# Performance work log

Hardware: AMD Instinct MI355X
Metric: run time of the kernel (lower is better)

Reference implementation:

```python
import jax, jax.numpy as jnp
import numpy as np


def setup_inputs() -> dict:
    key = jax.random.key(0)
    k1, k2, k3 = jax.random.split(key, 3)
    N, K, d, d_out = 100000, 32, 64, 64
    x = jax.random.normal(k1, (N, d), dtype=jnp.float32)
    edge_index = jax.random.randint(k2, (N, K), 0, N, dtype=jnp.int64)
    W = jax.random.normal(k3, (2 * d, d_out), dtype=jnp.float32) * (1.0 / np.sqrt(2 * d))
    b = jnp.zeros((d_out,), dtype=jnp.float32)
    return {"x": x, "edge_index": edge_index, "W": W, "b": b}


def reference(x, edge_index, W, b):
    # x: [N, d], edge_index: [N, K] dense neighbor indices
    x_j = x[edge_index]                                  # [N, K, d] gather
    # concat([x_i, x_j - x_i]) then max over K. The x_i half is constant over K,
    # so its max is x itself; max of the diff half computed directly (same math,
    # avoids materializing the [N, K, 2d] concat).
    diff_max = jnp.max(x_j - x[:, None, :], axis=1)      # [N, d]
    h = jnp.concatenate([x, diff_max], axis=-1)          # [N, 2d]
    return h @ W + b                                     # [N, d_out]
```

## Files before the change

### kernel.cpp

```cpp
#include <hip/hip_runtime.h>
#include <hip/hip_bf16.h>
#include <cstdint>


typedef __attribute__((ext_vector_type(8))) short short8;
typedef __attribute__((ext_vector_type(4))) float f4;

#define TILE 16
#define ROWS 168

__device__ __forceinline__ unsigned short f2bf(float f) {
  unsigned int u = __builtin_bit_cast(unsigned int, f);
  u += 0x7fffu + ((u >> 16) & 1u);
  return (unsigned short)(u >> 16);
}
__device__ __forceinline__ unsigned int pack2(float a, float b) {
  return (unsigned int)f2bf(a) | ((unsigned int)f2bf(b) << 16);
}
__device__ __forceinline__ float bflo(unsigned int u) {
  return __builtin_bit_cast(float, u << 16);
}
__device__ __forceinline__ float bfhi(unsigned int u) {
  return __builtin_bit_cast(float, u & 0xffff0000u);
}

__global__ __launch_bounds__(256)
void convert_kernel(const float* __restrict__ x, unsigned int* __restrict__ xbf,
                    const float* __restrict__ W, unsigned short* __restrict__ wf,
                    int n8, int nxb) {
  if ((int)blockIdx.x < nxb) {
    int i = blockIdx.x * 256 + threadIdx.x;
    if (i >= n8) return;
    const f4* p = (const f4*)x + (size_t)i * 2;
    f4 a = p[0], b = p[1];
    uint4 w;
    w.x = pack2(a.x, a.y); w.y = pack2(a.z, a.w);
    w.z = pack2(b.x, b.y); w.w = pack2(b.z, b.w);
    ((uint4*)xbf)[i] = w;
  } else {
    #pragma unroll
    for (int q = 0; q < 4; ++q) {
      int idx = threadIdx.x * 4 + q;
      int wv = idx >> 8, ks = (idx >> 6) & 3, l = idx & 63;
      int c = l & 15, g = l >> 4;
      short8 v;
      #pragma unroll
      for (int j = 0; j < 8; ++j)
        v[j] = (short)f2bf(W[(ks * 32 + g * 8 + j) * 64 + wv * 16 + c]);
      *(short8*)(wf + (size_t)idx * 8) = v;
    }
  }
}

__global__ __launch_bounds__(256, 6)
void mrconv3_kernel(const unsigned int* __restrict__ xbf,
                    const unsigned short* __restrict__ wf,
                    const int* __restrict__ ei,
                    const float* __restrict__ bias,
                    float* __restrict__ out,
                    int n_tiles)
{
  __shared__ __align__(16) unsigned short hs[TILE * ROWS];
  __shared__ __align__(16) int eis[TILE * 32];
  __shared__ __align__(16) float otile[TILE * 64];

  const int tid  = threadIdx.x;
  const int wv   = tid >> 6;
  const int lane = tid & 63;
  const int c = lane & 15;
  const int g = lane >> 4;
  const int t2 = lane >> 4;
  const int h  = (lane >> 3) & 1;
  const int e  = lane & 7;

  const int node0 = blockIdx.x * TILE;
  const int t = wv * 4 + t2;

  short8 bfrag[4];
  #pragma unroll
  for (int ks = 0; ks < 4; ++ks)
    bfrag[ks] = *(const short8*)(wf + (size_t)((wv * 4 + ks) * 64 + lane) * 8);

  *(int2*)&eis[tid * 2] = *(const int2*)(ei + (size_t)node0 * 32 + tid * 2);
  __syncthreads();

  const float NEG = -3.4e38f;
  const uint4 xr = *(const uint4*)(xbf + (size_t)(node0 + t) * 32 + e * 4);
  float l0 = NEG, h0 = NEG, l1 = NEG, h1 = NEG;
  float l2 = NEG, h2 = NEG, l3 = NEG, h3 = NEG;
  #pragma unroll
  for (int it = 0; it < 16; it += 2) {
    const int ja = eis[t * 32 + it * 2 + h];
    const int jb = eis[t * 32 + it * 2 + 2 + h];
    const uint4 ra = *(const uint4*)(xbf + (size_t)ja * 32 + e * 4);
    const uint4 rb = *(const uint4*)(xbf + (size_t)jb * 32 + e * 4);
    l0 = fmaxf(l0, fmaxf(bflo(ra.x), bflo(rb.x)));
    h0 = fmaxf(h0, fmaxf(bfhi(ra.x), bfhi(rb.x)));
    l1 = fmaxf(l1, fmaxf(bflo(ra.y), bflo(rb.y)));
    h1 = fmaxf(h1, fmaxf(bfhi(ra.y), bfhi(rb.y)));
    l2 = fmaxf(l2, fmaxf(bflo(ra.z), bflo(rb.z)));
    h2 = fmaxf(h2, fmaxf(bfhi(ra.z), bfhi(rb.z)));
    l3 = fmaxf(l3, fmaxf(bflo(ra.w), bflo(rb.w)));
    h3 = fmaxf(h3, fmaxf(bfhi(ra.w), bfhi(rb.w)));
  }
  l0 = fmaxf(l0, __shfl_xor(l0, 8));  h0 = fmaxf(h0, __shfl_xor(h0, 8));
  l1 = fmaxf(l1, __shfl_xor(l1, 8));  h1 = fmaxf(h1, __shfl_xor(h1, 8));
  l2 = fmaxf(l2, __shfl_xor(l2, 8));  h2 = fmaxf(h2, __shfl_xor(h2, 8));
  l3 = fmaxf(l3, __shfl_xor(l3, 8));  h3 = fmaxf(h3, __shfl_xor(h3, 8));

  if (h == 0) {
    uint4 w;
    w.x = pack2(l0 - bflo(xr.x), h0 - bfhi(xr.x));
    w.y = pack2(l1 - bflo(xr.y), h1 - bfhi(xr.y));
    w.z = pack2(l2 - bflo(xr.z), h2 - bfhi(xr.z));
    w.w = pack2(l3 - bflo(xr.w), h3 - bfhi(xr.w));
    *(uint4*)(hs + t * ROWS + 64 + e * 8) = w;
  } else {
    *(uint4*)(hs + t * ROWS + e * 8) = xr;
  }
  __syncthreads();

  f4 acc = {0.f, 0.f, 0.f, 0.f};
  #pragma unroll
  for (int ks = 0; ks < 4; ++ks) {
    short8 a = *(const short8*)(hs + c * ROWS + ks * 32 + g * 8);
    acc = __builtin_amdgcn_mfma_f32_16x16x32_bf16(a, bfrag[ks], acc, 0, 0, 0);
  }

  const float bb = bias[wv * 16 + c];
  #pragma unroll
  for (int j = 0; j < 4; ++j)
    otile[(g * 4 + j) * 64 + wv * 16 + c] = acc[j] + bb;
  __syncthreads();
  *(f4*)(out + (size_t)node0 * 64 + tid * 4) = *(const f4*)&otile[tid * 4];
}

#define FWPB 4
#define FROWS 160
__global__ __launch_bounds__(256, 4)
void mrconv_fp32_kernel(const float* __restrict__ x,
                        const int* __restrict__ ei,
                        const float* __restrict__ W,
                        const float* __restrict__ bias,
                        float* __restrict__ out,
                        int n_tiles)
{
  __shared__ __align__(16) unsigned short hsf[FWPB][TILE * FROWS];
  const int wave = threadIdx.x >> 6;
  const int lane = threadIdx.x & 63;
  const int c = lane & 15;
  const int g = lane >> 4;

  short8 bfrag[4][4];
  #pragma unroll
  for (int ks = 0; ks < 4; ++ks) {
    #pragma unroll
    for (int nt = 0; nt < 4; ++nt) {
      short8 v;
      #pragma unroll
      for (int j = 0; j < 8; ++j) {
        int k = ks * 32 + g * 8 + j;
        v[j] = (short)f2bf(W[k * 64 + nt * 16 + c]);
      }
      bfrag[ks][nt] = v;
    }
  }

  const int tile = blockIdx.x * FWPB + wave;
  if (tile >= n_tiles) return;
  const int node0 = tile * TILE;
  unsigned short* hrow = &hsf[wave][0];

  #pragma unroll 2
  for (int t = 0; t < TILE; ++t) {
    const int n = node0 + t;
    const f4 xi = *(const f4*)(x + (size_t)n * 64 + 4 * c);
    f4 m = { -3.4e38f, -3.4e38f, -3.4e38f, -3.4e38f };
    #pragma unroll
    for (int it = 0; it < 8; ++it) {
      const int j = ei[(size_t)n * 32 + it * 4 + g];
      const f4 xj = *(const f4*)(x + (size_t)j * 64 + 4 * c);
      m.x = fmaxf(m.x, xj.x - xi.x);
      m.y = fmaxf(m.y, xj.y - xi.y);
      m.z = fmaxf(m.z, xj.z - xi.z);
      m.w = fmaxf(m.w, xj.w - xi.w);
    }
    m.x = fmaxf(m.x, __shfl_xor(m.x, 16));
    m.y = fmaxf(m.y, __shfl_xor(m.y, 16));
    m.z = fmaxf(m.z, __shfl_xor(m.z, 16));
    m.w = fmaxf(m.w, __shfl_xor(m.w, 16));
    m.x = fmaxf(m.x, __shfl_xor(m.x, 32));
    m.y = fmaxf(m.y, __shfl_xor(m.y, 32));
    m.z = fmaxf(m.z, __shfl_xor(m.z, 32));
    m.w = fmaxf(m.w, __shfl_xor(m.w, 32));
    if (g == 0) {
      ushort4 p;
      p.x = f2bf(xi.x); p.y = f2bf(xi.y); p.z = f2bf(xi.z); p.w = f2bf(xi.w);
      *(ushort4*)(hrow + t * FROWS + 4 * c) = p;
    } else if (g == 1) {
      ushort4 p;
      p.x = f2bf(m.x); p.y = f2bf(m.y); p.z = f2bf(m.z); p.w = f2bf(m.w);
      *(ushort4*)(hrow + t * FROWS + 64 + 4 * c) = p;
    }
  }
  __asm__ volatile("s_waitcnt lgkmcnt(0)" ::: "memory");

  f4 acc[4] = {{0.f,0.f,0.f,0.f},{0.f,0.f,0.f,0.f},{0.f,0.f,0.f,0.f},{0.f,0.f,0.f,0.f}};
  #pragma unroll
  for (int ks = 0; ks < 4; ++ks) {
    short8 a = *(const short8*)(hrow + c * FROWS + ks * 32 + g * 8);
    #pragma unroll
    for (int nt = 0; nt < 4; ++nt)
      acc[nt] = __builtin_amdgcn_mfma_f32_16x16x32_bf16(a, bfrag[ks][nt], acc[nt], 0, 0, 0);
  }
  const int rbase = node0 + g * 4;
  #pragma unroll
  for (int nt = 0; nt < 4; ++nt) {
    const float bb = bias[nt * 16 + c];
    #pragma unroll
    for (int j = 0; j < 4; ++j)
      out[(size_t)(rbase + j) * 64 + nt * 16 + c] = acc[nt][j] + bb;
  }
}

extern "C" void kernel_launch(void* const* d_in, const int* in_sizes, int n_in,
                              void* d_out, int out_size, void* d_ws, size_t ws_size,
                              hipStream_t stream) {
  const float* x  = (const float*)d_in[0];
  const int*   ei = (const int*)d_in[1];
  const float* W  = (const float*)d_in[2];
  const float* b  = (const float*)d_in[3];
  float* out = (float*)d_out;

  const int N = in_sizes[0] / 64;
  const int n_tiles = N / TILE;

  const size_t xbf_bytes = (size_t)N * 64 * 2;
  const size_t wf_bytes  = 1024 * 16;
  if (ws_size >= xbf_bytes + wf_bytes) {
    unsigned int*   xbf = (unsigned int*)d_ws;
    unsigned short* wf  = (unsigned short*)((char*)d_ws + xbf_bytes);
    const int n8  = N * 64 / 8;
    const int nxb = (n8 + 255) / 256;
    hipLaunchKernelGGL(convert_kernel, dim3(nxb + 1), dim3(256), 0, stream,
                       x, xbf, W, wf, n8, nxb);
    hipLaunchKernelGGL(mrconv3_kernel, dim3(n_tiles), dim3(256), 0, stream,
                       xbf, wf, ei, b, out, n_tiles);
  } else {
    const int blocks = (n_tiles + FWPB - 1) / FWPB;
    hipLaunchKernelGGL(mrconv_fp32_kernel, dim3(blocks), dim3(256), 0, stream,
                       x, ei, W, b, out, n_tiles);
  }
}
```

Before: 129.9 us.

## Use order-preserving bf16 keys with packed u16 max and batch all neighbor gathers

The convert kernel now stores x in bf16 with an order-preserving key encoding. The main kernel can then reduce neighbors with packed unsigned 16-bit max instead of unpacking to float and using fmaxf. All 16 neighbor row loads per lane are issued up front behind a sched_barrier to raise memory-level parallelism, and edge indices are loaded as 64-bit words and de-interleaved into shared memory. Nontemporal loads and stores are added for streaming data, and the occupancy hint drops from 6 to 5, trading occupancy for the extra registers needed by the batched gathers.

```diff
diff --git a/kernel.cpp b/kernel.cpp
--- a/kernel.cpp
+++ b/kernel.cpp
@@ -5,6 +5,8 @@
 
 typedef __attribute__((ext_vector_type(8))) short short8;
 typedef __attribute__((ext_vector_type(4))) float f4;
+typedef __attribute__((ext_vector_type(8))) unsigned short u16x8;
+typedef __attribute__((ext_vector_type(4))) unsigned int u32x4;
 
 #define TILE 16
 #define ROWS 168
@@ -22,6 +24,19 @@
 }
 __device__ __forceinline__ float bfhi(unsigned int u) {
   return __builtin_bit_cast(float, u & 0xffff0000u);
+}
+__device__ __forceinline__ unsigned int key2(unsigned int u) {
+  unsigned int s = u & 0x80008000u;
+  unsigned int m = (s >> 15) * 0x7fffu;
+  return u ^ (0x80008000u | m);
+}
+__device__ __forceinline__ unsigned int unkey2(unsigned int k) {
+  unsigned int s = k & 0x80008000u;
+  unsigned int m = ((s >> 15) ^ 0x00010001u) * 0x7fffu;
+  return k ^ (0x80008000u | m);
+}
+__device__ __forceinline__ u16x8 pmax8(u16x8 a, u16x8 b) {
+  return __builtin_elementwise_max(a, b);
 }
 
 __global__ __launch_bounds__(256)
@@ -32,11 +47,12 @@
     int i = blockIdx.x * 256 + threadIdx.x;
     if (i >= n8) return;
     const f4* p = (const f4*)x + (size_t)i * 2;
-    f4 a = p[0], b = p[1];
-    uint4 w;
-    w.x = pack2(a.x, a.y); w.y = pack2(a.z, a.w);
-    w.z = pack2(b.x, b.y); w.w = pack2(b.z, b.w);
-    ((uint4*)xbf)[i] = w;
+    f4 a = __builtin_nontemporal_load(p);
+    f4 b = __builtin_nontemporal_load(p + 1);
+    u32x4 w;
+    w.x = key2(pack2(a.x, a.y)); w.y = key2(pack2(a.z, a.w));
+    w.z = key2(pack2(b.x, b.y)); w.w = key2(pack2(b.z, b.w));
+    __builtin_nontemporal_store(w, (u32x4*)xbf + i);
   } else {
     #pragma unroll
     for (int q = 0; q < 4; ++q) {
@@ -52,7 +68,7 @@
   }
 }
 
-__global__ __launch_bounds__(256, 6)
+__global__ __launch_bounds__(256, 5)
 void mrconv3_kernel(const unsigned int* __restrict__ xbf,
                     const unsigned short* __restrict__ wf,
                     const int* __restrict__ ei,
@@ -76,48 +92,69 @@
   const int node0 = blockIdx.x * TILE;
   const int t = wv * 4 + t2;
 
+  {
+    long long ev = __builtin_nontemporal_load(
+        (const long long*)ei + (size_t)node0 * 16 + tid);
+    const int ts = tid >> 4, qs = tid & 15;
+    eis[ts * 32 + qs]      = (int)ev;
+    eis[ts * 32 + 16 + qs] = (int)(ev >> 32);
+  }
+  __syncthreads();
+
+  const char* __restrict__ xb = (const char*)xbf;
+  const unsigned eoff = (unsigned)e * 16u;
+  const u16x8 xrk = *(const u16x8*)(xb + ((unsigned)(node0 + t) * 128u + eoff));
+
+  const int4* ip = (const int4*)&eis[(t * 2 + h) * 16];
+  const int4 i0 = ip[0], i1 = ip[1], i2 = ip[2], i3 = ip[3];
+  const int jj[16] = {i0.x, i0.y, i0.z, i0.w, i1.x, i1.y, i1.z, i1.w,
+                      i2.x, i2.y, i2.z, i2.w, i3.x, i3.y, i3.z, i3.w};
+  u16x8 r[16];
+  #pragma unroll
+  for (int q = 0; q < 16; ++q)
+    r[q] = *(const u16x8*)(xb + ((unsigned)jj[q] * 128u + eoff));
+  __builtin_amdgcn_sched_barrier(0);
+
+  u16x8 ka = pmax8(r[0], r[1]);
+  u16x8 kb = pmax8(r[2], r[3]);
+  #pragma unroll
+  for (int q = 4; q < 16; q += 4) {
+    ka = pmax8(ka, pmax8(r[q],     r[q + 1]));
+    kb = pmax8(kb, pmax8(r[q + 2], r[q + 3]));
+  }
+  u16x8 km = pmax8(ka, kb);
+
+  u32x4 k4 = __builtin_bit_cast(u32x4, km);
+  u32x4 s4;
+  s4.x = (unsigned)__shfl_xor((int)k4.x, 8);
+  s4.y = (unsigned)__shfl_xor((int)k4.y, 8);
+  s4.z = (unsigned)__shfl_xor((int)k4.z, 8);
+  s4.w = (unsigned)__shfl_xor((int)k4.w, 8);
+  km = pmax8(km, __builtin_bit_cast(u16x8, s4));
+  k4 = __builtin_bit_cast(u32x4, km);
+
+  const u32x4 xr4 = __builtin_bit_cast(u32x4, xrk);
+  u32x4 xw;
+  xw.x = unkey2(xr4.x); xw.y = unkey2(xr4.y);
+  xw.z = unkey2(xr4.z); xw.w = unkey2(xr4.w);
+
+  if (h == 0) {
+    const unsigned m0 = unkey2(k4.x), m1 = unkey2(k4.y);
+    const unsigned m2 = unkey2(k4.z), m3 = unkey2(k4.w);
+    u32x4 w;
+    w.x = pack2(bflo(m0) - bflo(xw.x), bfhi(m0) - bfhi(xw.x));
+    w.y = pack2(bflo(m1) - bflo(xw.y), bfhi(m1) - bfhi(xw.y));
+    w.z = pack2(bflo(m2) - bflo(xw.z), bfhi(m2) - bfhi(xw.z));
+    w.w = pack2(bflo(m3) - bflo(xw.w), bfhi(m3) - bfhi(xw.w));
+    *(u32x4*)(hs + t * ROWS + 64 + e * 8) = w;
+  } else {
+    *(u32x4*)(hs + t * ROWS + e * 8) = xw;
+  }
+
   short8 bfrag[4];
   #pragma unroll
   for (int ks = 0; ks < 4; ++ks)
     bfrag[ks] = *(const short8*)(wf + (size_t)((wv * 4 + ks) * 64 + lane) * 8);
-
-  *(int2*)&eis[tid * 2] = *(const int2*)(ei + (size_t)node0 * 32 + tid * 2);
-  __syncthreads();
-
-  const float NEG = -3.4e38f;
-  const uint4 xr = *(const uint4*)(xbf + (size_t)(node0 + t) * 32 + e * 4);
-  float l0 = NEG, h0 = NEG, l1 = NEG, h1 = NEG;
-  float l2 = NEG, h2 = NEG, l3 = NEG, h3 = NEG;
-  #pragma unroll
-  for (int it = 0; it < 16; it += 2) {
-    const int ja = eis[t * 32 + it * 2 + h];
-    const int jb = eis[t * 32 + it * 2 + 2 + h];
-    const uint4 ra = *(const uint4*)(xbf + (size_t)ja * 32 + e * 4);
-    const uint4 rb = *(const uint4*)(xbf + (size_t)jb * 32 + e * 4);
-    l0 = fmaxf(l0, fmaxf(bflo(ra.x), bflo(rb.x)));
-    h0 = fmaxf(h0, fmaxf(bfhi(ra.x), bfhi(rb.x)));
-    l1 = fmaxf(l1, fmaxf(bflo(ra.y), bflo(rb.y)));
-    h1 = fmaxf(h1, fmaxf(bfhi(ra.y), bfhi(rb.y)));
-    l2 = fmaxf(l2, fmaxf(bflo(ra.z), bflo(rb.z)));
-    h2 = fmaxf(h2, fmaxf(bfhi(ra.z), bfhi(rb.z)));
-    l3 = fmaxf(l3, fmaxf(bflo(ra.w), bflo(rb.w)));
-    h3 = fmaxf(h3, fmaxf(bfhi(ra.w), bfhi(rb.w)));
-  }
-  l0 = fmaxf(l0, __shfl_xor(l0, 8));  h0 = fmaxf(h0, __shfl_xor(h0, 8));
-  l1 = fmaxf(l1, __shfl_xor(l1, 8));  h1 = fmaxf(h1, __shfl_xor(h1, 8));
-  l2 = fmaxf(l2, __shfl_xor(l2, 8));  h2 = fmaxf(h2, __shfl_xor(h2, 8));
-  l3 = fmaxf(l3, __shfl_xor(l3, 8));  h3 = fmaxf(h3, __shfl_xor(h3, 8));
-
-  if (h == 0) {
-    uint4 w;
-    w.x = pack2(l0 - bflo(xr.x), h0 - bfhi(xr.x));
-    w.y = pack2(l1 - bflo(xr.y), h1 - bfhi(xr.y));
-    w.z = pack2(l2 - bflo(xr.z), h2 - bfhi(xr.z));
-    w.w = pack2(l3 - bflo(xr.w), h3 - bfhi(xr.w));
-    *(uint4*)(hs + t * ROWS + 64 + e * 8) = w;
-  } else {
-    *(uint4*)(hs + t * ROWS + e * 8) = xr;
-  }
   __syncthreads();
 
   f4 acc = {0.f, 0.f, 0.f, 0.f};
@@ -132,7 +169,8 @@
   for (int j = 0; j < 4; ++j)
     otile[(g * 4 + j) * 64 + wv * 16 + c] = acc[j] + bb;
   __syncthreads();
-  *(f4*)(out + (size_t)node0 * 64 + tid * 4) = *(const f4*)&otile[tid * 4];
+  __builtin_nontemporal_store(*(const f4*)&otile[tid * 4],
+                              (f4*)(out + (size_t)node0 * 64) + tid);
 }
 
 #define FWPB 4
```

Result: slower. 133.3 us (+2.6%).
